# Optimization experiments

Hardware: AMD Instinct MI355X
Metric: run time of the kernel (lower is better)

The kernel has to match this reference:

```python
import jax, jax.numpy as jnp
import numpy as np

NUM_GROUPS = 4
EPS = 1e-6


def group_norm(x, scale, bias):
    # x: [b, c, h, w]; GroupNorm32 computes stats in fp32 (x already fp32 here)
    b, c, h, w = x.shape
    xg = x.reshape(b, NUM_GROUPS, c // NUM_GROUPS, h, w)
    mean = jnp.mean(xg, axis=(2, 3, 4), keepdims=True)
    var = jnp.var(xg, axis=(2, 3, 4), keepdims=True)
    xn = ((xg - mean) * jax.lax.rsqrt(var + EPS)).reshape(b, c, h, w)
    return xn * scale[None, :, None, None] + bias[None, :, None, None]


def conv1x1(x, w, b):
    # 1x1 conv == channel mix: x [b,c,h,w], w [co,ci]
    return jnp.einsum('bchw,dc->bdhw', x, w) + b[None, :, None, None]


def setup_inputs() -> dict:
    key = jax.random.key(0)
    ks = jax.random.split(key, 6)
    c = 256
    s = 1.0 / np.sqrt(c)
    return {
        'x': jax.random.normal(ks[0], (4, c, 64, 64), dtype=jnp.float32),
        'gn_scale': jnp.ones((c,), jnp.float32),
        'gn_bias': jnp.zeros((c,), jnp.float32),
        'wq': jax.random.normal(ks[1], (c, c), jnp.float32) * s,
        'bq': jnp.zeros((c,), jnp.float32),
        'wk': jax.random.normal(ks[2], (c, c), jnp.float32) * s,
        'bk': jnp.zeros((c,), jnp.float32),
        'wv': jax.random.normal(ks[3], (c, c), jnp.float32) * s,
        'bv': jnp.zeros((c,), jnp.float32),
        'wproj': jax.random.normal(ks[4], (c, c), jnp.float32) * s,
        'bproj': jnp.zeros((c,), jnp.float32),
    }


def reference(x, gn_scale, gn_bias, wq, bq, wk, bk, wv, bv, wproj, bproj):
    b, c, h, w = x.shape
    hw = h * w
    h_ = group_norm(x, gn_scale, gn_bias)
    q = conv1x1(h_, wq, bq).reshape(b, c, hw)  # [b, c, hw]
    k = conv1x1(h_, wk, bk).reshape(b, c, hw)
    v = conv1x1(h_, wv, bv).reshape(b, c, hw)
    scale = jnp.float32(1.0 / np.sqrt(c))
    # attn[b, i, j] = sum_c q[b,c,i] * k[b,c,j], fp32 softmax over j
    attn = jnp.einsum('bci,bcj->bij', q.astype(jnp.float32), k.astype(jnp.float32)) * scale
    attn = jax.nn.softmax(attn, axis=-1).astype(x.dtype)
    # out[b, c, i] = sum_j v[b,c,j] * attn[b,i,j]
    out = jnp.einsum('bcj,bij->bci', v, attn).reshape(b, c, h, w)
    out = conv1x1(out, wproj, bproj)
    return x + out
```

## Files before the change

### kernel.cpp

```cpp
#include <hip/hip_runtime.h>


#define HW 4096
#define CCH 256
#define NBATCH 4
#define GN_N (64 * HW)

typedef unsigned short u16;
typedef __attribute__((ext_vector_type(8))) short bf16x8;
typedef __attribute__((ext_vector_type(4))) float f32x4;
typedef __attribute__((ext_vector_type(16))) float f32x16;
typedef __attribute__((ext_vector_type(4))) u16 u16x4;

__device__ __forceinline__ u16 f2bf(float f) {
  unsigned u = __float_as_uint(f);
  u += 0x7fffu + ((u >> 16) & 1u);
  return (u16)(u >> 16);
}
__device__ __forceinline__ float bf2f(u16 h) { return __uint_as_float(((unsigned)h) << 16); }

__device__ __forceinline__ void gload_lds16(const void* g, void* l) {
  __builtin_amdgcn_global_load_lds(
      (const __attribute__((address_space(1))) unsigned*)g,
      (__attribute__((address_space(3))) unsigned*)l, 16, 0, 0);
}

__global__ __launch_bounds__(256) void gn_partial(const float* __restrict__ x,
                                                  float* __restrict__ part) {
  const int bg = blockIdx.y, blk = blockIdx.x, tid = threadIdx.x;
  const float4* X = (const float4*)(x + (size_t)bg * GN_N);
  float s = 0.f, ss = 0.f;
#pragma unroll
  for (int u = 0; u < 8; ++u) {
    float4 v = X[blk * 2048 + u * 256 + tid];
    s += v.x + v.y + v.z + v.w;
    ss += v.x * v.x + v.y * v.y + v.z * v.z + v.w * v.w;
  }
  for (int off = 32; off; off >>= 1) { s += __shfl_xor(s, off); ss += __shfl_xor(ss, off); }
  __shared__ float rs[4], rss[4];
  const int w = tid >> 6;
  if ((tid & 63) == 0) { rs[w] = s; rss[w] = ss; }
  __syncthreads();
  if (tid == 0) {
    part[(bg * 32 + blk) * 2 + 0] = rs[0] + rs[1] + rs[2] + rs[3];
    part[(bg * 32 + blk) * 2 + 1] = rss[0] + rss[1] + rss[2] + rss[3];
  }
}

__global__ void gn_finalize(const float* __restrict__ part, float2* __restrict__ stats) {
  const int t = threadIdx.x;
  if (t < 16) {
    float s = 0.f, ss = 0.f;
    for (int u = 0; u < 32; ++u) { s += part[(t * 32 + u) * 2]; ss += part[(t * 32 + u) * 2 + 1]; }
    const float mean = s * (1.0f / GN_N);
    const float var = ss * (1.0f / GN_N) - mean * mean;
    stats[t] = make_float2(mean, rsqrtf(var + 1e-6f));
  }
}

__global__ __launch_bounds__(256) void norm_tr(const float* __restrict__ x,
                                               const float2* __restrict__ stats,
                                               const float* __restrict__ gsc,
                                               const float* __restrict__ gbi,
                                               u16* __restrict__ Ht) {
  __shared__ u16 T[64][72];
  const int i0 = blockIdx.x * 64, c0 = blockIdx.y * 64, b = blockIdx.z;
  const int tid = threadIdx.x;
  const int cl = tid >> 4;
  const int il4 = (tid & 15) * 4;
#pragma unroll
  for (int it = 0; it < 4; ++it) {
    const int c = c0 + it * 16 + cl;
    const float2 st = stats[b * 4 + (c >> 6)];
    const float sc = gsc[c] * st.y;
    const float bi = gbi[c] - st.x * sc;
    const float4 v = *(const float4*)&x[((size_t)(b * CCH + c)) * HW + i0 + il4];
    T[il4 + 0][it * 16 + cl] = f2bf(v.x * sc + bi);
    T[il4 + 1][it * 16 + cl] = f2bf(v.y * sc + bi);
    T[il4 + 2][it * 16 + cl] = f2bf(v.z * sc + bi);
    T[il4 + 3][it * 16 + cl] = f2bf(v.w * sc + bi);
  }
  __syncthreads();
  const int il = tid >> 2, cs = (tid & 3) * 16;
  const uint4 a = *(const uint4*)&T[il][cs];
  const uint4 b2 = *(const uint4*)&T[il][cs + 8];
  const size_t o = ((size_t)b * HW + i0 + il) * CCH + c0 + cs;
  *(uint4*)&Ht[o] = a;
  *(uint4*)&Ht[o + 8] = b2;
}

__global__ __launch_bounds__(256) void wcast(const float* __restrict__ w0, const float* __restrict__ w1,
                                             const float* __restrict__ w2, const float* __restrict__ w3,
                                             u16* __restrict__ dst) {
  const float* src = blockIdx.y == 0 ? w0 : blockIdx.y == 1 ? w1 : blockIdx.y == 2 ? w2 : w3;
  u16* d = dst + (size_t)blockIdx.y * 65536;
  const int idx = (blockIdx.x * 256 + threadIdx.x) * 8;
  const float4 a = *(const float4*)&src[idx];
  const float4 c = *(const float4*)&src[idx + 4];
  uint4 p;
  p.x = (unsigned)f2bf(a.x) | ((unsigned)f2bf(a.y) << 16);
  p.y = (unsigned)f2bf(a.z) | ((unsigned)f2bf(a.w) << 16);
  p.z = (unsigned)f2bf(c.x) | ((unsigned)f2bf(c.y) << 16);
  p.w = (unsigned)f2bf(c.z) | ((unsigned)f2bf(c.w) << 16);
  *(uint4*)&d[idx] = p;
}

template <int EPI, bool HASB>
__global__ __launch_bounds__(256) void gemm2(
    const u16* __restrict__ A, int lda, long sA,
    const u16* __restrict__ Bm, int ldb, long sB,
    void* __restrict__ O0, int ldo, long sO,
    void* __restrict__ O1, void* __restrict__ O2,
    const float* __restrict__ b0, const float* __restrict__ b1, const float* __restrict__ b2,
    const float* __restrict__ aux, long sAux,
    float scale, int K) {
  __shared__ char lsA[32768], lsB[32768];
  int bx, by, bz;
  {
    const int nx = gridDim.x, ny = gridDim.y;
    const int lin = blockIdx.x + nx * (blockIdx.y + ny * blockIdx.z);
    const int q = (nx * ny * (int)gridDim.z) >> 3;
    const int wg = (lin & 7) * q + (lin >> 3);
    bx = wg % nx; const int t2 = wg / nx; by = t2 % ny; bz = t2 / ny;
  }
  const int tid = threadIdx.x;
  const int w = tid >> 6, l = tid & 63;
  const int wm = w >> 1, wn = w & 1;
  const int m0 = by * 128, n0 = bx * 128;
  const u16* Ab = A + (size_t)bz * sA;
  const u16* Bb = Bm + (size_t)bz * sB;

  f32x4 acc[4][4];
#pragma unroll
  for (int i = 0; i < 4; ++i)
#pragma unroll
    for (int j = 0; j < 4; ++j)
#pragma unroll
      for (int q2 = 0; q2 < 4; ++q2) acc[i][j][q2] = 0.f;

  auto stage = [&](int buf, int k0) {
#pragma unroll
    for (int s = 0; s < 4; ++s) {
      const int o = s * 4096 + tid * 16;
      const int r = o >> 7;
      const int c = ((o >> 4) & 7) ^ (r & 7);
      const int ke = c * 8;
      gload_lds16(Ab + (size_t)(m0 + r) * lda + k0 + ke, lsA + buf * 16384 + s * 4096 + w * 1024);
      gload_lds16(Bb + (size_t)(n0 + r) * ldb + k0 + ke, lsB + buf * 16384 + s * 4096 + w * 1024);
    }
  };

  const int nt = K >> 6;
  stage(0, 0);
  asm volatile("s_waitcnt vmcnt(0)" ::: "memory");
  __syncthreads();
  for (int t = 0; t < nt; ++t) {
    const int cur = t & 1;
    if (t + 1 < nt) stage(cur ^ 1, (t + 1) << 6);
#pragma unroll
    for (int kk = 0; kk < 2; ++kk) {
      bf16x8 aF[4], bF[4];
#pragma unroll
      for (int mi = 0; mi < 4; ++mi) {
        const int r = wm * 64 + mi * 16 + (l & 15);
        const int cc = (kk * 4 + (l >> 4)) ^ (r & 7);
        aF[mi] = *(const bf16x8*)(lsA + cur * 16384 + r * 128 + cc * 16);
      }
#pragma unroll
      for (int ni = 0; ni < 4; ++ni) {
        const int r = wn * 64 + ni * 16 + (l & 15);
        const int cc = (kk * 4 + (l >> 4)) ^ (r & 7);
        bF[ni] = *(const bf16x8*)(lsB + cur * 16384 + r * 128 + cc * 16);
      }
#pragma unroll
      for (int mi = 0; mi < 4; ++mi)
#pragma unroll
        for (int ni = 0; ni < 4; ++ni)
          acc[mi][ni] = __builtin_amdgcn_mfma_f32_16x16x32_bf16(aF[mi], bF[ni], acc[mi][ni], 0, 0, 0);
    }
    asm volatile("s_waitcnt vmcnt(0)" ::: "memory");
    __syncthreads();
  }

  const int lc = l & 15;
  const int lr4 = (l >> 4) * 4;

  if (EPI == 5) {
    const int sel = m0 >> 8;
    const float* bs = sel == 0 ? b0 : sel == 1 ? b1 : b2;
#pragma unroll
    for (int mi = 0; mi < 4; ++mi) {
      const int mg = m0 + wm * 64 + mi * 16 + lr4;
      const int mloc = mg & 255;
      const float4 bv = *(const float4*)&bs[mloc];
      float bb4[4] = {bv.x, bv.y, bv.z, bv.w};
#pragma unroll
      for (int ni = 0; ni < 4; ++ni) {
        const int n = n0 + wn * 64 + ni * 16 + lc;
        if (sel == 2) {
          u16* V = (u16*)O2 + (size_t)bz * sO;
          const size_t vb = (size_t)(n >> 3) * 2048 + (n & 7);
#pragma unroll
          for (int q2 = 0; q2 < 4; ++q2)
            V[vb + (size_t)(mloc + q2) * 8] = f2bf(acc[mi][ni][q2] + bb4[q2]);
        } else {
          u16* Oq = (u16*)(sel == 0 ? O0 : O1) + (size_t)bz * sO;
          u16x4 pk;
#pragma unroll
          for (int q2 = 0; q2 < 4; ++q2) pk[q2] = f2bf(acc[mi][ni][q2] + bb4[q2]);
          *(u16x4*)&Oq[(size_t)n * CCH + mloc] = pk;
        }
      }
    }
  } else {
    float* O = (float*)O0 + (size_t)bz * sO;
    const float* R = aux + (size_t)bz * sAux;
#pragma unroll
    for (int mi = 0; mi < 4; ++mi) {
      const int mb = m0 + wm * 64 + mi * 16 + lr4;
      float bb4[4] = {0.f, 0.f, 0.f, 0.f};
      if (HASB) {
        const float4 bv = *(const float4*)&b0[mb];
        bb4[0] = bv.x; bb4[1] = bv.y; bb4[2] = bv.z; bb4[3] = bv.w;
      }
#pragma unroll
      for (int ni = 0; ni < 4; ++ni) {
        const int n = n0 + wn * 64 + ni * 16 + lc;
#pragma unroll
        for (int q2 = 0; q2 < 4; ++q2)
          O[(size_t)(mb + q2) * ldo + n] = acc[mi][ni][q2] * scale + bb4[q2] + R[(size_t)(mb + q2) * ldo + n];
      }
    }
  }
}

__global__ __launch_bounds__(256) void attn_fused(
    const u16* __restrict__ Qt, const u16* __restrict__ Kt, const u16* __restrict__ Vg,
    float* __restrict__ Opart, float* __restrict__ Rpart) {
  __shared__ __attribute__((aligned(16))) char lds[2][65536];
  __shared__ __attribute__((aligned(16))) unsigned P_block[64][36];
  const int bid = blockIdx.x;
  const int it = bid >> 3, b = (bid >> 1) & 3, jh = bid & 1;
  const int tid = threadIdx.x, w = tid >> 6, l = tid & 63;
  const int l31 = l & 31, h5 = l >> 5;
  const int jb = w >> 1, ib = w & 1;
  const u16* Qb = Qt + (size_t)b * HW * CCH;
  const u16* Kb = Kt + (size_t)b * HW * CCH;
  const u16* Vb = Vg + (size_t)b * HW * CCH;
  const int iw0 = it * 64;

  bf16x8 q[16];
#pragma unroll
  for (int kc = 0; kc < 16; ++kc)
    q[kc] = *(const bf16x8*)&Qb[(size_t)(iw0 + ib * 32 + l31) * CCH + kc * 16 + h5 * 8];

  f32x16 oacc[2][2];
#pragma unroll
  for (int i = 0; i < 2; ++i)
#pragma unroll
    for (int j = 0; j < 2; ++j)
#pragma unroll
      for (int r = 0; r < 16; ++r) oacc[i][j][r] = 0.f;
  float rsum = 0.f;

  auto stage = [&](int buf, int j0) {
    char* Kl = lds[buf];
    char* Vl = Kl + 32768;
#pragma unroll
    for (int s = 0; s < 16; ++s) {
      const int i = s * 4 + w;
      if (i < 32) {
        const int row = i * 2 + (l >> 5);
        const int c5 = l & 31;
        gload_lds16(Kb + (size_t)(j0 + row) * CCH + ((c5 ^ (row & 7)) * 8), Kl + i * 1024);
      } else {
        const int jj = i - 32;
        const int jg = jj >> 2, sub = jj & 3;
        const int cc = sub * 64 + l;
        gload_lds16(Vb + (size_t)((j0 >> 3) + jg) * 2048 + cc * 8, Vl + jg * 4096 + sub * 1024);
      }
    }
  };

  const int j0base = jh * 2048;
  const int NT = 32;
  stage(0, j0base);
  asm volatile("s_waitcnt vmcnt(0)" ::: "memory");
  __builtin_amdgcn_s_barrier();

  for (int t = 0; t < NT; ++t) {
    const int cur = t & 1;
    if (t + 1 < NT) stage(cur ^ 1, j0base + (t + 1) * 64);
    const char* Kl = lds[cur];
    const char* Vl = Kl + 32768;
    f32x16 sacc;
#pragma unroll
    for (int r = 0; r < 16; ++r) sacc[r] = 0.f;
    __builtin_amdgcn_s_setprio(1);
#pragma unroll
    for (int kc = 0; kc < 16; ++kc) {
      const int row = jb * 32 + l31;
      const int c5 = (kc * 2 + h5) ^ (row & 7);
      const bf16x8 kf = *(const bf16x8*)(Kl + row * 512 + c5 * 16);
      sacc = __builtin_amdgcn_mfma_f32_32x32x16_bf16(kf, q[kc], sacc, 0, 0, 0);
    }
    __builtin_amdgcn_s_setprio(0);
    {
      const int iL = ib * 32 + l31;
#pragma unroll
      for (int a = 0; a < 4; ++a) {
        const float p0 = __expf(sacc[4 * a + 0] * 0.0625f - 8.0f);
        const float p1 = __expf(sacc[4 * a + 1] * 0.0625f - 8.0f);
        const float p2 = __expf(sacc[4 * a + 2] * 0.0625f - 8.0f);
        const float p3 = __expf(sacc[4 * a + 3] * 0.0625f - 8.0f);
        const u16 e0 = f2bf(p0), e1 = f2bf(p1), e2 = f2bf(p2), e3 = f2bf(p3);
        rsum += (bf2f(e0) + bf2f(e1)) + (bf2f(e2) + bf2f(e3));
        *(uint2*)&P_block[iL][jb * 16 + 4 * a + 2 * h5] =
            make_uint2((unsigned)e0 | ((unsigned)e1 << 16),
                       (unsigned)e2 | ((unsigned)e3 << 16));
      }
    }
    asm volatile("s_waitcnt lgkmcnt(0)" ::: "memory");
    __builtin_amdgcn_sched_barrier(0);
    __builtin_amdgcn_s_barrier();
    __builtin_amdgcn_s_setprio(1);
#pragma unroll
    for (int js16 = 0; js16 < 4; ++js16) {
      bf16x8 af[2], vf[2];
#pragma unroll
      for (int itile = 0; itile < 2; ++itile)
        af[itile] = *(const bf16x8*)&P_block[itile * 32 + l31][js16 * 8 + h5 * 4];
#pragma unroll
      for (int ct = 0; ct < 2; ++ct) {
        const int c = w * 64 + ct * 32 + l31;
        vf[ct] = *(const bf16x8*)(Vl + (js16 * 2 + h5) * 4096 + c * 16);
      }
#pragma unroll
      for (int itile = 0; itile < 2; ++itile)
#pragma unroll
        for (int ct = 0; ct < 2; ++ct)
          oacc[itile][ct] = __builtin_amdgcn_mfma_f32_32x32x16_bf16(af[itile], vf[ct], oacc[itile][ct], 0, 0, 0);
    }
    __builtin_amdgcn_s_setprio(0);
    asm volatile("s_waitcnt vmcnt(0) lgkmcnt(0)" ::: "memory");
    __builtin_amdgcn_sched_barrier(0);
    __builtin_amdgcn_s_barrier();
  }

  rsum += __shfl_xor(rsum, 32);
  if (l < 32)
    Rpart[(size_t)(jh * 2 + jb) * 16384 + b * HW + iw0 + ib * 32 + l31] = rsum;
  float* Op = Opart + (size_t)jh * 16384 * CCH + (size_t)b * HW * CCH + (size_t)iw0 * CCH;
#pragma unroll
  for (int itile = 0; itile < 2; ++itile)
#pragma unroll
    for (int ct = 0; ct < 2; ++ct) {
      const int c = w * 64 + ct * 32 + l31;
#pragma unroll
      for (int r = 0; r < 16; ++r) {
        const int row = itile * 32 + (r & 3) + 8 * (r >> 2) + 4 * h5;
        Op[(size_t)row * CCH + c] = oacc[itile][ct][r];
      }
    }
}

__global__ __launch_bounds__(256) void attn_combine(const float* __restrict__ Op,
                                                    const float* __restrict__ Rp,
                                                    u16* __restrict__ Ot) {
  const int idx = blockIdx.x * 256 + threadIdx.x;
  const int row = idx >> 6;
  const int c4 = (idx & 63) * 4;
  const float4 o0 = *(const float4*)&Op[(size_t)row * CCH + c4];
  const float4 o1 = *(const float4*)&Op[(size_t)16384 * CCH + (size_t)row * CCH + c4];
  float rs = 0.f;
#pragma unroll
  for (int s = 0; s < 4; ++s) rs += Rp[(size_t)s * 16384 + row];
  const float inv = 1.0f / rs;
  u16x4 r;
  r[0] = f2bf((o0.x + o1.x) * inv);
  r[1] = f2bf((o0.y + o1.y) * inv);
  r[2] = f2bf((o0.z + o1.z) * inv);
  r[3] = f2bf((o0.w + o1.w) * inv);
  *(u16x4*)&Ot[(size_t)row * CCH + c4] = r;
}

extern "C" void kernel_launch(void* const* d_in, const int* in_sizes, int n_in,
                              void* d_out, int out_size, void* d_ws, size_t ws_size,
                              hipStream_t stream) {
  const float* x   = (const float*)d_in[0];
  const float* gsc = (const float*)d_in[1];
  const float* gbi = (const float*)d_in[2];
  const float* wq  = (const float*)d_in[3];
  const float* bq  = (const float*)d_in[4];
  const float* wk  = (const float*)d_in[5];
  const float* bk  = (const float*)d_in[6];
  const float* wv  = (const float*)d_in[7];
  const float* bv  = (const float*)d_in[8];
  const float* wp  = (const float*)d_in[9];
  const float* bp  = (const float*)d_in[10];
  float* out = (float*)d_out;

  char* ws = (char*)d_ws;
  size_t off = 0;
  auto alloc = [&](size_t bytes) {
    size_t o = off; off = (off + bytes + 255) & ~(size_t)255; return o;
  };
  const size_t szMat = (size_t)NBATCH * HW * CCH * 2;
  u16* W      = (u16*)(ws + alloc(4 * 65536 * 2));
  float* pgn  = (float*)(ws + alloc(16 * 32 * 2 * 4));
  float2* st  = (float2*)(ws + alloc(16 * 8));
  u16* Ht = (u16*)(ws + alloc(szMat));
  u16* Qt = (u16*)(ws + alloc(szMat));
  u16* Kt = (u16*)(ws + alloc(szMat));
  u16* Vg = (u16*)(ws + alloc(szMat));
  u16* Ot = (u16*)(ws + alloc(szMat));
  float* Opart = (float*)(ws + alloc((size_t)2 * 16384 * CCH * 4));
  float* Rpart = (float*)(ws + alloc((size_t)4 * 16384 * 4));

  const long sM = (long)HW * CCH;

  wcast<<<dim3(32, 4), 256, 0, stream>>>(wq, wk, wv, wp, W);
  gn_partial<<<dim3(32, 16), 256, 0, stream>>>(x, pgn);
  gn_finalize<<<1, 64, 0, stream>>>(pgn, st);
  norm_tr<<<dim3(HW / 64, CCH / 64, NBATCH), 256, 0, stream>>>(x, st, gsc, gbi, Ht);

  gemm2<5, true><<<dim3(32, 6, NBATCH), 256, 0, stream>>>(
      W, 256, 0, Ht, 256, sM, Qt, 256, sM, Kt, Vg, bq, bk, bv, nullptr, 0, 1.f, 256);

  attn_fused<<<512, 256, 0, stream>>>(Qt, Kt, Vg, Opart, Rpart);
  attn_combine<<<4096, 256, 0, stream>>>(Opart, Rpart, Ot);

  gemm2<2, true><<<dim3(32, 2, NBATCH), 256, 0, stream>>>(
      W + 3 * 65536, 256, 0, Ot, 256, sM, out, HW, (long)CCH * HW, nullptr, nullptr,
      bp, nullptr, nullptr, x, (long)CCH * HW, 1.f, 256);
}
```

Baseline: 188.6 us.

## Single-buffer K/V in LDS with split staging and dual QK accumulators

Replaces the double-buffered 128KB K/V LDS staging with a single 64KB buffer. The next tile's K is loaded during the PV MFMA phase and its V after PV finishes, with an extra barrier between them. The halved LDS footprint is meant to allow two blocks per CU so that the other block hides load latency. The QK reduction is split into two independent MFMA accumulator chains to shorten the dependency chain. In exchange, the V load is no longer overlapped within the block and extra synchronization is added.

```diff
diff --git a/kernel.cpp b/kernel.cpp
--- a/kernel.cpp
+++ b/kernel.cpp
@@ -237,7 +237,7 @@
 __global__ __launch_bounds__(256) void attn_fused(
     const u16* __restrict__ Qt, const u16* __restrict__ Kt, const u16* __restrict__ Vg,
     float* __restrict__ Opart, float* __restrict__ Rpart) {
-  __shared__ __attribute__((aligned(16))) char lds[2][65536];
+  __shared__ __attribute__((aligned(16))) char lds[65536];
   __shared__ __attribute__((aligned(16))) unsigned P_block[64][36];
   const int bid = blockIdx.x;
   const int it = bid >> 3, b = (bid >> 1) & 3, jh = bid & 1;
@@ -263,48 +263,55 @@
       for (int r = 0; r < 16; ++r) oacc[i][j][r] = 0.f;
   float rsum = 0.f;
 
-  auto stage = [&](int buf, int j0) {
-    char* Kl = lds[buf];
-    char* Vl = Kl + 32768;
-#pragma unroll
-    for (int s = 0; s < 16; ++s) {
+  auto stageK = [&](int j0) {
+#pragma unroll
+    for (int s = 0; s < 8; ++s) {
       const int i = s * 4 + w;
-      if (i < 32) {
-        const int row = i * 2 + (l >> 5);
-        const int c5 = l & 31;
-        gload_lds16(Kb + (size_t)(j0 + row) * CCH + ((c5 ^ (row & 7)) * 8), Kl + i * 1024);
-      } else {
-        const int jj = i - 32;
-        const int jg = jj >> 2, sub = jj & 3;
-        const int cc = sub * 64 + l;
-        gload_lds16(Vb + (size_t)((j0 >> 3) + jg) * 2048 + cc * 8, Vl + jg * 4096 + sub * 1024);
-      }
+      const int row = i * 2 + (l >> 5);
+      const int c5 = l & 31;
+      gload_lds16(Kb + (size_t)(j0 + row) * CCH + ((c5 ^ (row & 7)) * 8), lds + i * 1024);
+    }
+  };
+  auto stageV = [&](int j0) {
+    char* Vl = lds + 32768;
+#pragma unroll
+    for (int s = 0; s < 8; ++s) {
+      const int jj = s * 4 + w;
+      const int jg = jj >> 2, sub = jj & 3;
+      const int cc = sub * 64 + l;
+      gload_lds16(Vb + (size_t)((j0 >> 3) + jg) * 2048 + cc * 8, Vl + jg * 4096 + sub * 1024);
     }
   };
 
   const int j0base = jh * 2048;
   const int NT = 32;
-  stage(0, j0base);
+  stageK(j0base);
+  stageV(j0base);
   asm volatile("s_waitcnt vmcnt(0)" ::: "memory");
   __builtin_amdgcn_s_barrier();
 
   for (int t = 0; t < NT; ++t) {
-    const int cur = t & 1;
-    if (t + 1 < NT) stage(cur ^ 1, j0base + (t + 1) * 64);
-    const char* Kl = lds[cur];
-    const char* Vl = Kl + 32768;
+    const int j0n = j0base + (t + 1) * 64;
+    const char* Kl = lds;
+    const char* Vl = lds + 32768;
+    f32x16 s0, s1;
+#pragma unroll
+    for (int r = 0; r < 16; ++r) { s0[r] = 0.f; s1[r] = 0.f; }
+    __builtin_amdgcn_s_setprio(1);
+#pragma unroll
+    for (int kc = 0; kc < 16; kc += 2) {
+      const int row = jb * 32 + l31;
+      const int c5a = (kc * 2 + h5) ^ (row & 7);
+      const int c5b = ((kc + 1) * 2 + h5) ^ (row & 7);
+      const bf16x8 kf0 = *(const bf16x8*)(Kl + row * 512 + c5a * 16);
+      const bf16x8 kf1 = *(const bf16x8*)(Kl + row * 512 + c5b * 16);
+      s0 = __builtin_amdgcn_mfma_f32_32x32x16_bf16(kf0, q[kc], s0, 0, 0, 0);
+      s1 = __builtin_amdgcn_mfma_f32_32x32x16_bf16(kf1, q[kc + 1], s1, 0, 0, 0);
+    }
+    __builtin_amdgcn_s_setprio(0);
     f32x16 sacc;
 #pragma unroll
-    for (int r = 0; r < 16; ++r) sacc[r] = 0.f;
-    __builtin_amdgcn_s_setprio(1);
-#pragma unroll
-    for (int kc = 0; kc < 16; ++kc) {
-      const int row = jb * 32 + l31;
-      const int c5 = (kc * 2 + h5) ^ (row & 7);
-      const bf16x8 kf = *(const bf16x8*)(Kl + row * 512 + c5 * 16);
-      sacc = __builtin_amdgcn_mfma_f32_32x32x16_bf16(kf, q[kc], sacc, 0, 0, 0);
-    }
-    __builtin_amdgcn_s_setprio(0);
+    for (int r = 0; r < 16; ++r) sacc[r] = s0[r] + s1[r];
     {
       const int iL = ib * 32 + l31;
 #pragma unroll
@@ -323,6 +330,7 @@
     asm volatile("s_waitcnt lgkmcnt(0)" ::: "memory");
     __builtin_amdgcn_sched_barrier(0);
     __builtin_amdgcn_s_barrier();
+    if (t + 1 < NT) stageK(j0n);
     __builtin_amdgcn_s_setprio(1);
 #pragma unroll
     for (int js16 = 0; js16 < 4; ++js16) {
@@ -342,7 +350,11 @@
           oacc[itile][ct] = __builtin_amdgcn_mfma_f32_32x32x16_bf16(af[itile], vf[ct], oacc[itile][ct], 0, 0, 0);
     }
     __builtin_amdgcn_s_setprio(0);
-    asm volatile("s_waitcnt vmcnt(0) lgkmcnt(0)" ::: "memory");
+    asm volatile("s_waitcnt lgkmcnt(0)" ::: "memory");
+    __builtin_amdgcn_sched_barrier(0);
+    __builtin_amdgcn_s_barrier();
+    if (t + 1 < NT) stageV(j0n);
+    asm volatile("s_waitcnt vmcnt(0)" ::: "memory");
     __builtin_amdgcn_sched_barrier(0);
     __builtin_amdgcn_s_barrier();
   }
```

New measurement: 197.6 us. +4.8%, slower.
